# Kernel optimization log

Hardware: AMD Instinct MI355X
Metric: run time of the kernel (lower is better)

Reference implementation:

```python
import jax, jax.numpy as jnp
import numpy as np

DIM = 16
NUM_SPECIES = 10
CUTOFF = 5.0
NUM_CONVS = 3
N_ATM = 131072
N_BND = 1048576
N_ANG = 2097152
N_GRAPHS = 256
PI = 3.141592653589793


def _bessel(x, end, num_basis):
    # Sinusoidal (Bessel) radial basis on (0, end]. x: [E] -> [E, num_basis]
    xx = x[:, None] + 1e-5
    n = jnp.arange(1, num_basis + 1, dtype=x.dtype)
    return jnp.sqrt(2.0 / end) * jnp.sin(n * PI * xx / end) / xx


def _gaussian(x, start, end, num_basis):
    centers = jnp.linspace(start, end, num_basis).astype(x.dtype)
    gamma = 1.0 / (centers[1] - centers[0])
    return jnp.exp(-(gamma * (x[:, None] - centers)) ** 2)


def _ln(x, g, b):
    mu = jnp.mean(x, -1, keepdims=True)
    var = jnp.var(x, -1, keepdims=True)
    return (x - mu) * jax.lax.rsqrt(var + 1e-5) * g + b


def _embed(feat, W1, b1, W2, b2, g, b):
    # MLP([in, dim, dim], SiLU) + LayerNorm
    h = jax.nn.silu(feat @ W1 + b1)
    return _ln(h @ W2 + b2, g, b)


def _egconv(x, e, src, dst, W, bvec, lnp):
    # Edge-gated graph convolution (ALIGNN layer).
    # W: [5, D, D] = (W_src, W_dst, W_e, W_self, W_nbr); bvec: [2, D]; lnp: [2, 2, D]
    z = x[src] @ W[0] + x[dst] @ W[1] + e @ W[2] + bvec[0]  # [E, D]
    sigma = jax.nn.sigmoid(z)
    msg = sigma * (x[src] @ W[4])
    num = jax.ops.segment_sum(msg, dst, num_segments=x.shape[0])
    den = jax.ops.segment_sum(sigma, dst, num_segments=x.shape[0])
    x_new = x + jax.nn.silu(_ln(x @ W[3] + bvec[1] + num / (den + 1e-5), lnp[0, 0], lnp[0, 1]))
    e_new = e + jax.nn.silu(_ln(z, lnp[1, 0], lnp[1, 1]))
    return x_new, e_new


def _forward(x_atm, x_bnd, x_ang, mask_dih_ang, edge_index_G, edge_index_A, x_atm_batch,
             forcepair, enc_W1, enc_b1, enc_W2, enc_b2, enc_ln_g, enc_ln_b,
             conv_W, conv_b, conv_ln, l1_W, l1_b, l2_W, l2_b):
    # ---- Encoder ----
    # atom species one-hot, zero-padded from NUM_SPECIES to DIM columns (extra W rows unused)
    atm_feat = jax.nn.one_hot(x_atm, DIM, dtype=enc_W1.dtype)
    h_atm = _embed(atm_feat, enc_W1[0], enc_b1[0], enc_W2[0], enc_b2[0], enc_ln_g[0], enc_ln_b[0])
    h_bnd = _embed(_bessel(x_bnd, CUTOFF, DIM), enc_W1[1], enc_b1[1], enc_W2[1], enc_b2[1], enc_ln_g[1], enc_ln_b[1])
    h_ang_b = _embed(_gaussian(x_ang, 0.0, PI, DIM), enc_W1[2], enc_b1[2], enc_W2[2], enc_b2[2], enc_ln_g[2], enc_ln_b[2])
    h_ang_d = _embed(_gaussian(x_ang, -PI, PI, DIM), enc_W1[3], enc_b1[3], enc_W2[3], enc_b2[3], enc_ln_g[3], enc_ln_b[3])
    h_ang = jnp.where(mask_dih_ang[:, None], h_ang_d, h_ang_b)  # dihedral=True branch
    # ---- Processor: interleaved line-graph / atom-graph edge-gated convs ----
    srcA, dstA = edge_index_A[0], edge_index_A[1]
    srcG, dstG = edge_index_G[0], edge_index_G[1]
    for c in range(NUM_CONVS):
        h_bnd, h_ang = _egconv(h_bnd, h_ang, srcA, dstA, conv_W[c, 0], conv_b[c, 0], conv_ln[c, 0])
        h_atm, h_bnd = _egconv(h_atm, h_bnd, srcG, dstG, conv_W[c, 1], conv_b[c, 1], conv_ln[c, 1])
    # ---- Decoder: sum-pool atoms per graph ----
    h_pooled = jax.ops.segment_sum(h_atm, x_atm_batch, num_segments=N_GRAPHS)  # [G, D]
    # ---- Head ----
    x = jnp.concatenate([h_pooled, forcepair.reshape(N_GRAPHS, 2)], axis=-1)  # [G, D+2]
    x = jax.nn.leaky_relu(x @ l1_W + l1_b, negative_slope=0.01)
    return x @ l2_W + l2_b  # [G, 1]


def setup_inputs() -> dict:
    key = jax.random.key(0)
    ks = jax.random.split(key, 16)
    f32 = jnp.float32
    s = 0.25
    inp = {}
    inp["x_atm"] = jax.random.randint(ks[0], (N_ATM,), 0, NUM_SPECIES)
    inp["x_bnd"] = jax.random.uniform(ks[1], (N_BND,), f32, 0.5, CUTOFF)
    inp["x_ang"] = jax.random.uniform(ks[2], (N_ANG,), f32, -PI, PI)
    inp["mask_dih_ang"] = jax.random.randint(ks[3], (N_ANG,), 0, 2).astype(bool)
    inp["edge_index_G"] = jax.random.randint(ks[4], (2, N_BND), 0, N_ATM)
    inp["edge_index_A"] = jax.random.randint(ks[5], (2, N_ANG), 0, N_BND)
    inp["x_atm_batch"] = jnp.sort(jax.random.randint(ks[6], (N_ATM,), 0, N_GRAPHS))
    inp["forcepair"] = jax.random.normal(ks[7], (N_GRAPHS * 2,), f32)
    inp["enc_W1"] = jax.random.normal(ks[8], (4, DIM, DIM), f32) * s
    inp["enc_b1"] = jnp.zeros((4, DIM), f32)
    inp["enc_W2"] = jax.random.normal(ks[9], (4, DIM, DIM), f32) * s
    inp["enc_b2"] = jnp.zeros((4, DIM), f32)
    inp["enc_ln_g"] = jnp.ones((4, DIM), f32)
    inp["enc_ln_b"] = jnp.zeros((4, DIM), f32)
    inp["conv_W"] = jax.random.normal(ks[10], (NUM_CONVS, 2, 5, DIM, DIM), f32) * s
    inp["conv_b"] = jnp.zeros((NUM_CONVS, 2, 2, DIM), f32)
    inp["conv_ln"] = jnp.stack([jnp.ones((NUM_CONVS, 2, 2, DIM), f32), jnp.zeros((NUM_CONVS, 2, 2, DIM), f32)], axis=3)  # [C,2,2(node/edge? no: gamma/beta at axis 3)] -> [C,2,2,2,D]
    inp["l1_W"] = jax.random.normal(ks[11], (DIM + 2, DIM), f32) * s
    inp["l1_b"] = jnp.zeros((DIM,), f32)
    inp["l2_W"] = jax.random.normal(ks[12], (DIM, 1), f32) * s
    inp["l2_b"] = jnp.zeros((1,), f32)
    return inp


def reference(x_atm, x_bnd, x_ang, mask_dih_ang, edge_index_G, edge_index_A, x_atm_batch,
              forcepair, enc_W1, enc_b1, enc_W2, enc_b2, enc_ln_g, enc_ln_b,
              conv_W, conv_b, conv_ln, l1_W, l1_b, l2_W, l2_b):
    return _forward(x_atm, x_bnd, x_ang, mask_dih_ang, edge_index_G, edge_index_A, x_atm_batch,
                    forcepair, enc_W1, enc_b1, enc_W2, enc_b2, enc_ln_g, enc_ln_b,
                    conv_W, conv_b, conv_ln, l1_W, l1_b, l2_W, l2_b)
```

## Files before the change

### kernel.cpp

```cpp
#include <hip/hip_runtime.h>
#include <hip/hip_bf16.h>

#define N_ATM 131072
#define N_BND 1048576
#define N_ANG 2097152
#define N_GRAPHS 256
#define D_SPLIT (N_BND / 2)
#define CAP_SLOTS (N_ANG / 2 + 16384)
#define PI_F 3.14159265358979323846f

typedef __hip_bfloat16 bf16;

__device__ __forceinline__ int clampi(int v, int lo, int hi) {
    return v < lo ? lo : (v > hi ? hi : v);
}
__device__ __forceinline__ float b2f(bf16 v) { return __bfloat162float(v); }
__device__ __forceinline__ float sigmoidf_(float x) { return 1.0f / (1.0f + __expf(-x)); }
__device__ __forceinline__ float siluf_(float x) { return x / (1.0f + __expf(-x)); }

__device__ __forceinline__ float loadF(const void* p, long long i, int isbf) {
    return isbf ? b2f(((const bf16*)p)[i]) : ((const float*)p)[i];
}
__device__ __forceinline__ float bfbits2f(unsigned lo16) {
    union { unsigned u; float f; } c; c.u = lo16 << 16; return c.f;
}
__device__ __forceinline__ unsigned f2bfbits(float f) {
    union { float f; unsigned u; } c; c.f = f;
    unsigned u = c.u + 0x7FFFu + ((c.u >> 16) & 1u);
    return u >> 16;
}

__device__ __forceinline__ void load16f(const float* p, float* r) {
    const float4* q = (const float4*)p;
#pragma unroll
    for (int i = 0; i < 4; i++) { float4 v = q[i]; r[4*i]=v.x; r[4*i+1]=v.y; r[4*i+2]=v.z; r[4*i+3]=v.w; }
}
__device__ __forceinline__ void store16f(float* p, const float* r) {
    float4* q = (float4*)p;
#pragma unroll
    for (int i = 0; i < 4; i++) q[i] = make_float4(r[4*i], r[4*i+1], r[4*i+2], r[4*i+3]);
}
__device__ __forceinline__ void load16b(const bf16* p, float* r) {
    uint4 a = ((const uint4*)p)[0];
    uint4 b = ((const uint4*)p)[1];
    unsigned w[8] = {a.x, a.y, a.z, a.w, b.x, b.y, b.z, b.w};
#pragma unroll
    for (int i = 0; i < 8; i++) {
        r[2*i] = bfbits2f(w[i] & 0xFFFFu);
        union { unsigned u; float f; } c; c.u = w[i] & 0xFFFF0000u;
        r[2*i+1] = c.f;
    }
}
__device__ __forceinline__ void store16b(bf16* p, const float* r) {
    unsigned w[8];
#pragma unroll
    for (int i = 0; i < 8; i++)
        w[i] = f2bfbits(r[2*i]) | (f2bfbits(r[2*i+1]) << 16);
    ((uint4*)p)[0] = make_uint4(w[0], w[1], w[2], w[3]);
    ((uint4*)p)[1] = make_uint4(w[4], w[5], w[6], w[7]);
}

__global__ void __launch_bounds__(256) k_zero_int(int* __restrict__ p, int n) {
    int i = blockIdx.x * 256 + threadIdx.x;
    if (i < n) p[i] = 0;
}

__global__ void __launch_bounds__(256) k_detect(const void* lng, const unsigned* __restrict__ mask,
                                                int* flags) {
    int i = blockIdx.x * 256 + threadIdx.x;
    if (i == 0) flags[0] = (*(const unsigned*)lng == 0x3F803F80u) ? 1 : 0;
    int bad = 0;
    for (int j = i; j < 512 * 1024; j += 512 * 256)
        if (mask[j] > 1u) bad = 1;
    if (bad) atomicOr(&flags[1], 1);
}

__global__ void k_cvt_any(const void* __restrict__ src, float* __restrict__ dst, int n,
                          const int* __restrict__ flags) {
    int i = blockIdx.x * blockDim.x + threadIdx.x;
    if (i < n) dst[i] = loadF(src, i, flags[0]);
}

__global__ void __launch_bounds__(256) k_count(const int* __restrict__ dst, int* __restrict__ cnt,
                                               int E, int n) {
    int i = blockIdx.x * 256 + threadIdx.x;
    if (i >= E) return;
    atomicAdd(&cnt[clampi(dst[i], 0, n - 1)], 1);
}
__global__ void __launch_bounds__(256) k_scan_local(const int* __restrict__ cnt, int* __restrict__ ofs,
                                                    int* __restrict__ bsum, int n) {
    __shared__ int s[256];
    int t = threadIdx.x, i = blockIdx.x * 256 + t;
    int v = (i < n) ? cnt[i] : 0;
    s[t] = v; __syncthreads();
    for (int o = 1; o < 256; o <<= 1) {
        int add = (t >= o) ? s[t - o] : 0;
        __syncthreads();
        s[t] += add;
        __syncthreads();
    }
    if (i < n) ofs[i] = s[t] - v;
    if (t == 255) bsum[blockIdx.x] = s[255];
}
__global__ void __launch_bounds__(256) k_scan_bsum(int* __restrict__ bsum, int nb) {
    __shared__ int s[256];
    __shared__ int run;
    int t = threadIdx.x;
    if (t == 0) run = 0;
    __syncthreads();
    for (int base = 0; base < nb; base += 256) {
        int i = base + t;
        int v = (i < nb) ? bsum[i] : 0;
        s[t] = v; __syncthreads();
        for (int o = 1; o < 256; o <<= 1) {
            int add = (t >= o) ? s[t - o] : 0;
            __syncthreads();
            s[t] += add;
            __syncthreads();
        }
        if (i < nb) bsum[i] = run + s[t] - v;
        __syncthreads();
        if (t == 0) run += s[255];
        __syncthreads();
    }
}
__global__ void __launch_bounds__(256) k_scan_add(int* __restrict__ ofs, const int* __restrict__ bsum,
                                                  int* __restrict__ cursor, int n) {
    int i = blockIdx.x * 256 + threadIdx.x;
    if (i < n) { int v = ofs[i] + bsum[blockIdx.x]; ofs[i] = v; cursor[i] = v; }
}
__global__ void __launch_bounds__(256) k_scatter_line(
    const int* __restrict__ src, const int* __restrict__ dst, int* __restrict__ cur,
    int* __restrict__ srcP, int* __restrict__ dstP, int* __restrict__ pos, int E, int n)
{
    int i = blockIdx.x * 256 + threadIdx.x;
    if (i >= E) return;
    int d = clampi(dst[i], 0, n - 1);
    int s = clampi(src[i], 0, n - 1);
    int p = clampi(atomicAdd(&cur[d], 1), 0, E - 1);
    srcP[p] = s; dstP[p] = d; pos[i] = p;
}
__global__ void __launch_bounds__(256) k_scatter_pos(
    const int* __restrict__ dst, int* __restrict__ cur, int* __restrict__ pos, int E, int n)
{
    int i = blockIdx.x * 256 + threadIdx.x;
    if (i >= E) return;
    int d = clampi(dst[i], 0, n - 1);
    pos[i] = clampi(atomicAdd(&cur[d], 1), 0, E - 1);
}

__global__ void __launch_bounds__(256) k_enc_atm(
    const int* __restrict__ sp_in,
    const void* W1, const void* b1, const void* W2, const void* b2,
    const void* g, const void* be, const int* __restrict__ flags,
    float* __restrict__ out)
{
    __shared__ float sW1[256], sW2[256], sb1[16], sb2[16], sg[16], sbe[16];
    int t = threadIdx.x, isbf = flags[0];
    sW1[t] = loadF(W1, t, isbf); sW2[t] = loadF(W2, t, isbf);
    if (t < 16) { sb1[t]=loadF(b1,t,isbf); sb2[t]=loadF(b2,t,isbf); sg[t]=loadF(g,t,isbf); sbe[t]=loadF(be,t,isbf); }
    __syncthreads();
    int i = blockIdx.x * 256 + t;
    if (i >= N_ATM) return;
    int sp = clampi(sp_in[i], 0, 15);
    float h[16];
#pragma unroll
    for (int j = 0; j < 16; j++) h[j] = siluf_(sW1[sp * 16 + j] + sb1[j]);
    float o[16]; float mu = 0.f;
#pragma unroll
    for (int j = 0; j < 16; j++) {
        float a = sb2[j];
#pragma unroll
        for (int k = 0; k < 16; k++) a += h[k] * sW2[k * 16 + j];
        o[j] = a; mu += a;
    }
    mu *= (1.f / 16.f);
    float var = 0.f;
#pragma unroll
    for (int j = 0; j < 16; j++) { float d = o[j] - mu; var += d * d; }
    var *= (1.f / 16.f);
    float r = rsqrtf(var + 1e-5f);
    float ov[16];
#pragma unroll
    for (int j = 0; j < 16; j++) ov[j] = (o[j] - mu) * r * sg[j] + sbe[j];
    store16f(out + (long long)i * 16, ov);
}

__global__ void __launch_bounds__(256) k_enc_bnd(
    const void* __restrict__ xb,
    const void* W1, const void* b1, const void* W2, const void* b2,
    const void* g, const void* be, const int* __restrict__ flags,
    bf16* __restrict__ out)
{
    __shared__ float sW1[256], sW2[256], sb1[16], sb2[16], sg[16], sbe[16];
    int t = threadIdx.x, isbf = flags[0];
    sW1[t] = loadF(W1, 256 + t, isbf); sW2[t] = loadF(W2, 256 + t, isbf);
    if (t < 16) { sb1[t]=loadF(b1,16+t,isbf); sb2[t]=loadF(b2,16+t,isbf); sg[t]=loadF(g,16+t,isbf); sbe[t]=loadF(be,16+t,isbf); }
    __syncthreads();
    int i = blockIdx.x * 256 + t;
    if (i >= N_BND) return;
    float x = loadF(xb, i, isbf) + 1e-5f;
    const float c = 0.6324555320336759f;
    float inv = c / x;
    float feat[16];
#pragma unroll
    for (int k = 0; k < 16; k++) feat[k] = __sinf((float)(k + 1) * PI_F * x * 0.2f) * inv;
    float h[16];
#pragma unroll
    for (int j = 0; j < 16; j++) {
        float a = sb1[j];
#pragma unroll
        for (int k = 0; k < 16; k++) a += feat[k] * sW1[k * 16 + j];
        h[j] = siluf_(a);
    }
    float o[16]; float mu = 0.f;
#pragma unroll
    for (int j = 0; j < 16; j++) {
        float a = sb2[j];
#pragma unroll
        for (int k = 0; k < 16; k++) a += h[k] * sW2[k * 16 + j];
        o[j] = a; mu += a;
    }
    mu *= (1.f / 16.f);
    float var = 0.f;
#pragma unroll
    for (int j = 0; j < 16; j++) { float d = o[j] - mu; var += d * d; }
    var *= (1.f / 16.f);
    float r = rsqrtf(var + 1e-5f);
    float ov[16];
#pragma unroll
    for (int j = 0; j < 16; j++) ov[j] = (o[j] - mu) * r * sg[j] + sbe[j];
    store16b(out + (long long)i * 16, ov);
}

__global__ void __launch_bounds__(256) k_enc_ang(
    const void* __restrict__ xa, const void* __restrict__ mask,
    const void* W1, const void* b1, const void* W2, const void* b2,
    const void* g, const void* be, const int* __restrict__ flags,
    const int* __restrict__ pos, bf16* __restrict__ out)
{
    __shared__ float sW1[512], sW2[512], sb1[32], sb2[32], sg[32], sbe[32];
    int t = threadIdx.x, isbf = flags[0], mbyte = flags[1];
    for (int i = t; i < 512; i += 256) { sW1[i] = loadF(W1, 512 + i, isbf); sW2[i] = loadF(W2, 512 + i, isbf); }
    if (t < 32) { sb1[t]=loadF(b1,32+t,isbf); sb2[t]=loadF(b2,32+t,isbf); sg[t]=loadF(g,32+t,isbf); sbe[t]=loadF(be,32+t,isbf); }
    __syncthreads();
    int i = blockIdx.x * 256 + t;
    if (i >= N_ANG) return;
    int m = mbyte ? (((const unsigned char*)mask)[i] != 0) : (((const int*)mask)[i] != 0);
    float x = loadF(xa, i, isbf);
    float gam = m ? 2.3873241463784303f : 4.7746482927568605f;
    float c0  = m ? -PI_F : 0.0f;
    float dc  = m ? 0.41887902047863906f : 0.20943951023931953f;
    int wo = m * 256, vo = m * 16;
    float feat[16];
#pragma unroll
    for (int k = 0; k < 16; k++) {
        float d = gam * (x - (c0 + (float)k * dc));
        feat[k] = __expf(-d * d);
    }
    float h[16];
#pragma unroll
    for (int j = 0; j < 16; j++) {
        float a = sb1[vo + j];
#pragma unroll
        for (int k = 0; k < 16; k++) a += feat[k] * sW1[wo + k * 16 + j];
        h[j] = siluf_(a);
    }
    float o[16]; float mu = 0.f;
#pragma unroll
    for (int j = 0; j < 16; j++) {
        float a = sb2[vo + j];
#pragma unroll
        for (int k = 0; k < 16; k++) a += h[k] * sW2[wo + k * 16 + j];
        o[j] = a; mu += a;
    }
    mu *= (1.f / 16.f);
    float var = 0.f;
#pragma unroll
    for (int j = 0; j < 16; j++) { float d = o[j] - mu; var += d * d; }
    var *= (1.f / 16.f);
    float r = rsqrtf(var + 1e-5f);
    float ov[16];
#pragma unroll
    for (int j = 0; j < 16; j++) ov[j] = (o[j] - mu) * r * sg[vo + j] + sbe[vo + j];
    store16b(out + (long long)clampi(pos[i], 0, N_ANG - 1) * 16, ov);
}

__device__ __forceinline__ void edge_core(
    const float* xs, const float* xd, const float* ev,
    const float* sW, const float* sB, const float* sLg, const float* sLb,
    float* eo, unsigned* wpk)
{
    float z[16], mm[16];
#pragma unroll
    for (int j = 0; j < 16; j++) { z[j] = sB[j]; mm[j] = 0.f; }
#pragma unroll
    for (int k = 0; k < 16; k++) {
        float a = xs[k], c = xd[k], q = ev[k];
#pragma unroll
        for (int j = 0; j < 16; j++) {
            z[j] += a * sW[k * 16 + j] + c * sW[256 + k * 16 + j] + q * sW[512 + k * 16 + j];
            mm[j] += a * sW[1024 + k * 16 + j];
        }
    }
    float mu = 0.f;
#pragma unroll
    for (int j = 0; j < 16; j++) mu += z[j];
    mu *= (1.f / 16.f);
    float var = 0.f;
#pragma unroll
    for (int j = 0; j < 16; j++) { float dd = z[j] - mu; var += dd * dd; }
    var *= (1.f / 16.f);
    float r = rsqrtf(var + 1e-5f);
#pragma unroll
    for (int j = 0; j < 16; j++)
        eo[j] = ev[j] + siluf_((z[j] - mu) * r * sLg[j] + sLb[j]);
#pragma unroll
    for (int i = 0; i < 8; i++) {
        float a0 = sigmoidf_(z[2*i]);
        float a1 = sigmoidf_(z[2*i+1]);
        wpk[i]     = f2bfbits(a0 * mm[2*i]) | (f2bfbits(a1 * mm[2*i+1]) << 16);
        wpk[8 + i] = f2bfbits(a0)           | (f2bfbits(a1) << 16);
    }
}

__global__ void __launch_bounds__(256) k_econv_perm(
    const bf16* __restrict__ x, bf16* __restrict__ e,
    const int* __restrict__ srcP, const int* __restrict__ dstP,
    const float* __restrict__ W, const float* __restrict__ B, const float* __restrict__ L,
    bf16* __restrict__ scratch, const int* __restrict__ loP, const int* __restrict__ hiP,
    int E, int nn)
{
    int blk0 = blockIdx.x * 256;
    int lo = loP ? *loP : 0;
    int hi = hiP ? *hiP : E;
    if (blk0 + 256 <= lo || blk0 >= hi) return;
    __shared__ float sW[1280], sB[16], sLg[16], sLb[16];
    int t = threadIdx.x;
    for (int i = t; i < 1280; i += 256) sW[i] = W[i];
    if (t < 16) { sB[t] = B[t]; sLg[t] = L[32 + t]; sLb[t] = L[48 + t]; }
    __syncthreads();
    int p = blk0 + t;
    if (p < lo || p >= hi || p >= E) return;
    int s = clampi(srcP[p], 0, nn - 1);
    int d = clampi(dstP[p], 0, nn - 1);
    float xs[16], xd[16], ev[16];
    load16b(x + (long long)s * 16, xs);
    load16b(x + (long long)d * 16, xd);
    load16b(e + (long long)p * 16, ev);
    float eo[16]; unsigned wpk[16];
    edge_core(xs, xd, ev, sW, sB, sLg, sLb, eo, wpk);
    store16b(e + (long long)p * 16, eo);
    int slot = clampi(p - lo, 0, CAP_SLOTS - 1);
    uint4* sp4 = (uint4*)(scratch + (long long)slot * 32);
    sp4[0] = make_uint4(wpk[0],  wpk[1],  wpk[2],  wpk[3]);
    sp4[1] = make_uint4(wpk[4],  wpk[5],  wpk[6],  wpk[7]);
    sp4[2] = make_uint4(wpk[8],  wpk[9],  wpk[10], wpk[11]);
    sp4[3] = make_uint4(wpk[12], wpk[13], wpk[14], wpk[15]);
}

__global__ void __launch_bounds__(256) k_econv_nat(
    const float* __restrict__ x, bf16* __restrict__ e,
    const int* __restrict__ src, const int* __restrict__ dst, const int* __restrict__ pos,
    const float* __restrict__ W, const float* __restrict__ B, const float* __restrict__ L,
    bf16* __restrict__ scratch, int E, int nn)
{
    __shared__ float sW[1280], sB[16], sLg[16], sLb[16];
    int t = threadIdx.x;
    for (int i = t; i < 1280; i += 256) sW[i] = W[i];
    if (t < 16) { sB[t] = B[t]; sLg[t] = L[32 + t]; sLb[t] = L[48 + t]; }
    __syncthreads();
    int i = blockIdx.x * 256 + t;
    if (i >= E) return;
    int s = clampi(src[i], 0, nn - 1);
    int d = clampi(dst[i], 0, nn - 1);
    float xs[16], xd[16], ev[16];
    load16f(x + (long long)s * 16, xs);
    load16f(x + (long long)d * 16, xd);
    load16b(e + (long long)i * 16, ev);
    float eo[16]; unsigned wpk[16];
    edge_core(xs, xd, ev, sW, sB, sLg, sLb, eo, wpk);
    store16b(e + (long long)i * 16, eo);
    int slot = clampi(pos[i], 0, E - 1);
    uint4* sp4 = (uint4*)(scratch + (long long)slot * 32);
    sp4[0] = make_uint4(wpk[0],  wpk[1],  wpk[2],  wpk[3]);
    sp4[1] = make_uint4(wpk[4],  wpk[5],  wpk[6],  wpk[7]);
    sp4[2] = make_uint4(wpk[8],  wpk[9],  wpk[10], wpk[11]);
    sp4[3] = make_uint4(wpk[12], wpk[13], wpk[14], wpk[15]);
}

template <typename TX>
__device__ __forceinline__ void loadRow(const TX* p, float* r);
template <> __device__ __forceinline__ void loadRow<float>(const float* p, float* r) { load16f(p, r); }
template <> __device__ __forceinline__ void loadRow<bf16>(const bf16* p, float* r) { load16b(p, r); }
template <typename TX>
__device__ __forceinline__ void storeRow(TX* p, const float* r);
template <> __device__ __forceinline__ void storeRow<float>(float* p, const float* r) { store16f(p, r); }
template <> __device__ __forceinline__ void storeRow<bf16>(bf16* p, const float* r) { store16b(p, r); }

template <typename TX>
__global__ void __launch_bounds__(256) k_nconv(
    const TX* __restrict__ xo, TX* __restrict__ xn,
    const int* __restrict__ ofs, const int* __restrict__ endo,
    const float* __restrict__ W, const float* __restrict__ B, const float* __restrict__ L,
    const bf16* __restrict__ scratch, const int* __restrict__ baseP,
    int dlo, int dhi, int Emax, int cap)
{
    __shared__ float sW[256], sB[16], sLg[16], sLb[16];
    int t = threadIdx.x;
    sW[t] = W[768 + t];
    if (t < 16) { sB[t] = B[16 + t]; sLg[t] = L[t]; sLb[t] = L[16 + t]; }
    __syncthreads();
    int d = dlo + blockIdx.x * 256 + t;
    if (d >= dhi) return;
    int base = baseP ? *baseP : 0;
    float xv[16];
    loadRow<TX>(xo + (long long)d * 16, xv);
    float num[16], den[16];
#pragma unroll
    for (int j = 0; j < 16; j++) { num[j] = 0.f; den[j] = 0.f; }
    int p0 = clampi(ofs[d], 0, Emax);
    int p1 = clampi(endo[d], p0, Emax);
    for (int p = p0; p < p1; p++) {
        int idx = clampi(p - base, 0, cap - 1);
        const uint4* q = (const uint4*)(scratch + (long long)idx * 32);
        uint4 q0 = q[0], q1 = q[1], q2 = q[2], q3 = q[3];
        unsigned w[16] = {q0.x,q0.y,q0.z,q0.w, q1.x,q1.y,q1.z,q1.w,
                          q2.x,q2.y,q2.z,q2.w, q3.x,q3.y,q3.z,q3.w};
#pragma unroll
        for (int i = 0; i < 8; i++) {
            num[2*i]   += bfbits2f(w[i] & 0xFFFFu);
            num[2*i+1] += bfbits2f(w[i] >> 16);
            den[2*i]   += bfbits2f(w[8+i] & 0xFFFFu);
            den[2*i+1] += bfbits2f(w[8+i] >> 16);
        }
    }
    float tt[16]; float mu = 0.f;
#pragma unroll
    for (int j = 0; j < 16; j++) {
        float a = sB[j] + num[j] / (den[j] + 1e-5f);
#pragma unroll
        for (int k = 0; k < 16; k++) a += xv[k] * sW[k * 16 + j];
        tt[j] = a; mu += a;
    }
    mu *= (1.f / 16.f);
    float var = 0.f;
#pragma unroll
    for (int j = 0; j < 16; j++) { float dd = tt[j] - mu; var += dd * dd; }
    var *= (1.f / 16.f);
    float r = rsqrtf(var + 1e-5f);
    float ov[16];
#pragma unroll
    for (int j = 0; j < 16; j++)
        ov[j] = xv[j] + siluf_((tt[j] - mu) * r * sLg[j] + sLb[j]);
    storeRow<TX>(xn + (long long)d * 16, ov);
}

__global__ void __launch_bounds__(256) k_pool2(
    const float* __restrict__ h, const int* __restrict__ batch, float* __restrict__ pooled)
{
    int g = blockIdx.x;
    int lo = 0, hi = N_ATM;
    while (lo < hi) { int m = (lo + hi) >> 1; if (batch[m] < g) lo = m + 1; else hi = m; }
    int s0 = lo;
    lo = 0; hi = N_ATM;
    while (lo < hi) { int m = (lo + hi) >> 1; if (batch[m] < g + 1) lo = m + 1; else hi = m; }
    int s1 = lo;
    float acc[16];
#pragma unroll
    for (int j = 0; j < 16; j++) acc[j] = 0.f;
    for (int i = s0 + threadIdx.x; i < s1; i += 256) {
        float v[16];
        load16f(h + (long long)i * 16, v);
#pragma unroll
        for (int j = 0; j < 16; j++) acc[j] += v[j];
    }
#pragma unroll
    for (int j = 0; j < 16; j++)
        for (int o = 32; o > 0; o >>= 1) acc[j] += __shfl_down(acc[j], o, 64);
    __shared__ float red[4][16];
    int wv = threadIdx.x >> 6, ln = threadIdx.x & 63;
    if (ln == 0)
#pragma unroll
        for (int j = 0; j < 16; j++) red[wv][j] = acc[j];
    __syncthreads();
    if (threadIdx.x < 16)
        pooled[g * 16 + threadIdx.x] = red[0][threadIdx.x] + red[1][threadIdx.x]
                                     + red[2][threadIdx.x] + red[3][threadIdx.x];
}

__global__ void __launch_bounds__(256) k_head(
    const float* __restrict__ pooled, const void* __restrict__ fp,
    const void* l1W, const void* l1b, const void* l2W, const void* l2b,
    const int* __restrict__ flags, void* __restrict__ out)
{
    __shared__ float sW[18 * 16], sb[16], s2W[16];
    int t = threadIdx.x, isbf = flags[0];
    for (int i = t; i < 288; i += 256) sW[i] = loadF(l1W, i, isbf);
    if (t < 16) { sb[t] = loadF(l1b, t, isbf); s2W[t] = loadF(l2W, t, isbf); }
    __syncthreads();
    int g = t;
    if (g >= N_GRAPHS) return;
    float in[18];
#pragma unroll
    for (int j = 0; j < 16; j++) in[j] = pooled[g * 16 + j];
    in[16] = loadF(fp, 2 * g, isbf);
    in[17] = loadF(fp, 2 * g + 1, isbf);
    float acc = loadF(l2b, 0, isbf);
#pragma unroll
    for (int j = 0; j < 16; j++) {
        float h = sb[j];
#pragma unroll
        for (int k = 0; k < 18; k++) h += in[k] * sW[k * 16 + j];
        h = (h > 0.f) ? h : 0.01f * h;
        acc += h * s2W[j];
    }
    if (isbf) ((bf16*)out)[g] = __float2bfloat16(acc);
    else      ((float*)out)[g] = acc;
}

extern "C" void kernel_launch(void* const* d_in, const int* in_sizes, int n_in,
                              void* d_out, int out_size, void* d_ws, size_t ws_size,
                              hipStream_t stream) {
    const int*  x_atm = (const int*)d_in[0];
    const void* x_bnd = d_in[1];
    const void* x_ang = d_in[2];
    const void* mask  = d_in[3];
    const int*  eiG   = (const int*)d_in[4];
    const int*  eiA   = (const int*)d_in[5];
    const int*  batch = (const int*)d_in[6];
    const void* fp    = d_in[7];
    const void* eW1 = d_in[8],  *eb1 = d_in[9],  *eW2 = d_in[10], *eb2 = d_in[11];
    const void* elg = d_in[12], *elb = d_in[13];
    const void* convW = d_in[14], *convB = d_in[15], *convLN = d_in[16];
    const void* l1W = d_in[17], *l1b = d_in[18], *l2W = d_in[19], *l2b = d_in[20];

    const size_t NA16 = (size_t)N_ATM * 16;
    const size_t NB16 = (size_t)N_BND * 16;
    const size_t NG16 = (size_t)N_ANG * 16;

    char* p = (char*)d_ws;
    int*   flags  = (int*)p;   p += 256;
    float* cw     = (float*)p; p += 7680 * 4;
    float* cb     = (float*)p; p += 192 * 4;
    float* cln    = (float*)p; p += 384 * 4;
    float* pooled = (float*)p; p += 4096 * 4;
    int*   bsum   = (int*)p;   p += 4096 * 4;
    int*   cntB   = (int*)p;   p += (size_t)N_BND * 4;
    int*   ofsB   = (int*)p;   p += (size_t)N_BND * 4;
    int*   srcB   = (int*)p;   p += (size_t)N_ANG * 4;
    int*   dstB   = (int*)p;   p += (size_t)N_ANG * 4;
    int*   cntA   = (int*)p;   p += (size_t)N_ATM * 4;
    int*   ofsA   = (int*)p;   p += (size_t)N_ATM * 4;
    int*   posG   = (int*)p;   p += (size_t)N_BND * 4;
    float* h_atm  = (float*)p; p += NA16 * 4;
    bf16*  h_bndX = (bf16*)p;  p += NB16 * 2;
    bf16*  h_bndY = (bf16*)p;  p += NB16 * 2;
    bf16*  h_ang  = (bf16*)p;  p += NG16 * 2;
    int*   posB    = (int*)p;
    bf16*  scratch = (bf16*)p;

    k_zero_int<<<1, 64, 0, stream>>>(flags, 64);
    k_detect<<<512, 256, 0, stream>>>(elg, (const unsigned*)mask, flags);
    k_cvt_any<<<30, 256, 0, stream>>>(convW, cw, 7680, flags);
    k_cvt_any<<<1, 256, 0, stream>>>(convB, cb, 192, flags);
    k_cvt_any<<<2, 256, 0, stream>>>(convLN, cln, 384, flags);

    k_zero_int<<<N_BND / 256, 256, 0, stream>>>(cntB, N_BND);
    k_count<<<N_ANG / 256, 256, 0, stream>>>(eiA + N_ANG, cntB, N_ANG, N_BND);
    k_scan_local<<<N_BND / 256, 256, 0, stream>>>(cntB, ofsB, bsum, N_BND);
    k_scan_bsum<<<1, 256, 0, stream>>>(bsum, N_BND / 256);
    k_scan_add<<<N_BND / 256, 256, 0, stream>>>(ofsB, bsum, cntB, N_BND);
    k_scatter_line<<<N_ANG / 256, 256, 0, stream>>>(eiA, eiA + N_ANG, cntB, srcB, dstB, posB,
                                                    N_ANG, N_BND);
    k_zero_int<<<N_ATM / 256, 256, 0, stream>>>(cntA, N_ATM);
    k_count<<<N_BND / 256, 256, 0, stream>>>(eiG + N_BND, cntA, N_BND, N_ATM);
    k_scan_local<<<N_ATM / 256, 256, 0, stream>>>(cntA, ofsA, bsum, N_ATM);
    k_scan_bsum<<<1, 256, 0, stream>>>(bsum, N_ATM / 256);
    k_scan_add<<<N_ATM / 256, 256, 0, stream>>>(ofsA, bsum, cntA, N_ATM);
    k_scatter_pos<<<N_BND / 256, 256, 0, stream>>>(eiG + N_BND, cntA, posG, N_BND, N_ATM);

    k_enc_atm<<<N_ATM / 256, 256, 0, stream>>>(x_atm, eW1, eb1, eW2, eb2, elg, elb, flags, h_atm);
    k_enc_bnd<<<N_BND / 256, 256, 0, stream>>>(x_bnd, eW1, eb1, eW2, eb2, elg, elb, flags, h_bndX);
    k_enc_ang<<<N_ANG / 256, 256, 0, stream>>>(x_ang, mask, eW1, eb1, eW2, eb2, elg, elb, flags,
                                               posB, h_ang);

    bf16* X = h_bndX;
    bf16* Y = h_bndY;
    const int* split = ofsB + D_SPLIT;
    for (int c = 0; c < 3; c++) {
        const float* Wl = cw + (size_t)(c * 2 + 0) * 1280;
        const float* Bl = cb + (size_t)(c * 2 + 0) * 32;
        const float* Ll = cln + (size_t)(c * 2 + 0) * 64;
        k_econv_perm<<<N_ANG / 256, 256, 0, stream>>>(X, h_ang, srcB, dstB, Wl, Bl, Ll,
                                                      scratch, (const int*)nullptr, split,
                                                      N_ANG, N_BND);
        k_nconv<bf16><<<D_SPLIT / 256, 256, 0, stream>>>(X, Y, ofsB, cntB, Wl, Bl, Ll,
                                                         scratch, (const int*)nullptr,
                                                         0, D_SPLIT, N_ANG, CAP_SLOTS);
        k_econv_perm<<<N_ANG / 256, 256, 0, stream>>>(X, h_ang, srcB, dstB, Wl, Bl, Ll,
                                                      scratch, split, (const int*)nullptr,
                                                      N_ANG, N_BND);
        k_nconv<bf16><<<(N_BND - D_SPLIT) / 256, 256, 0, stream>>>(X, Y, ofsB, cntB, Wl, Bl, Ll,
                                                                   scratch, split,
                                                                   D_SPLIT, N_BND, N_ANG, CAP_SLOTS);
        const float* Wa = cw + (size_t)(c * 2 + 1) * 1280;
        const float* Ba = cb + (size_t)(c * 2 + 1) * 32;
        const float* La = cln + (size_t)(c * 2 + 1) * 64;
        k_econv_nat<<<N_BND / 256, 256, 0, stream>>>(h_atm, Y, eiG, eiG + N_BND, posG,
                                                     Wa, Ba, La, scratch, N_BND, N_ATM);
        k_nconv<float><<<N_ATM / 256, 256, 0, stream>>>(h_atm, h_atm, ofsA, cntA, Wa, Ba, La,
                                                        scratch, (const int*)nullptr,
                                                        0, N_ATM, N_BND, N_BND);
        bf16* tmp = X; X = Y; Y = tmp;
    }

    k_pool2<<<N_GRAPHS, 256, 0, stream>>>(h_atm, batch, pooled);
    k_head<<<1, 256, 0, stream>>>(pooled, fp, l1W, l1b, l2W, l2b, flags, d_out);
}
```

Before: 2.537 ms.

## Fuse edge and node convolution into one CSR-windowed kernel with shared-memory messages

Replaces the separate edge-conv and node-aggregation kernels with one fused kernel per conv. Each block handles a window of 256 destination-sorted edges (plus up to 64 extension edges), stages the packed sigma-message pairs in shared memory, and reduces them into the destination nodes it owns. This removes the global scratch round trip and the half-split launches. The atom graph now uses a CSR permutation with an edge-id indirection, which makes the bond-feature accesses indirect. Nodes with more incoming edges than the window's extension can hold would be aggregated incorrectly, and the owner/first ranges need extra binary-search setup kernels.

```diff
diff --git a/kernel.cpp b/kernel.cpp
--- a/kernel.cpp
+++ b/kernel.cpp
@@ -5,9 +5,11 @@
 #define N_BND 1048576
 #define N_ANG 2097152
 #define N_GRAPHS 256
-#define D_SPLIT (N_BND / 2)
-#define CAP_SLOTS (N_ANG / 2 + 16384)
 #define PI_F 3.14159265358979323846f
+
+#define FMAIN 256
+#define FEXT 64
+#define FWIN (FMAIN + FEXT)
 
 typedef __hip_bfloat16 bf16;
 
@@ -59,6 +61,15 @@
     ((uint4*)p)[0] = make_uint4(w[0], w[1], w[2], w[3]);
     ((uint4*)p)[1] = make_uint4(w[4], w[5], w[6], w[7]);
 }
+
+template <typename TX>
+__device__ __forceinline__ void loadRow(const TX* p, float* r);
+template <> __device__ __forceinline__ void loadRow<float>(const float* p, float* r) { load16f(p, r); }
+template <> __device__ __forceinline__ void loadRow<bf16>(const bf16* p, float* r) { load16b(p, r); }
+template <typename TX>
+__device__ __forceinline__ void storeRow(TX* p, const float* r);
+template <> __device__ __forceinline__ void storeRow<float>(float* p, const float* r) { store16f(p, r); }
+template <> __device__ __forceinline__ void storeRow<bf16>(bf16* p, const float* r) { store16b(p, r); }
 
 __global__ void __launch_bounds__(256) k_zero_int(int* __restrict__ p, int n) {
     int i = blockIdx.x * 256 + threadIdx.x;
@@ -124,29 +135,45 @@
         __syncthreads();
     }
 }
-__global__ void __launch_bounds__(256) k_scan_add(int* __restrict__ ofs, const int* __restrict__ bsum,
-                                                  int* __restrict__ cursor, int n) {
+__global__ void __launch_bounds__(256) k_scan_add2(int* __restrict__ ofs, const int* __restrict__ bsum,
+                                                   int* __restrict__ cursor, int n, int total) {
     int i = blockIdx.x * 256 + threadIdx.x;
     if (i < n) { int v = ofs[i] + bsum[blockIdx.x]; ofs[i] = v; cursor[i] = v; }
-}
-__global__ void __launch_bounds__(256) k_scatter_line(
+    if (i == 0) ofs[n] = total;
+}
+__global__ void __launch_bounds__(256) k_scatter_line2(
     const int* __restrict__ src, const int* __restrict__ dst, int* __restrict__ cur,
-    int* __restrict__ srcP, int* __restrict__ dstP, int* __restrict__ pos, int E, int n)
+    int* __restrict__ srcP, int* __restrict__ pos, int E, int n)
 {
     int i = blockIdx.x * 256 + threadIdx.x;
     if (i >= E) return;
     int d = clampi(dst[i], 0, n - 1);
     int s = clampi(src[i], 0, n - 1);
     int p = clampi(atomicAdd(&cur[d], 1), 0, E - 1);
-    srcP[p] = s; dstP[p] = d; pos[i] = p;
-}
-__global__ void __launch_bounds__(256) k_scatter_pos(
-    const int* __restrict__ dst, int* __restrict__ cur, int* __restrict__ pos, int E, int n)
+    srcP[p] = s; pos[i] = p;
+}
+__global__ void __launch_bounds__(256) k_scatter_atom2(
+    const int* __restrict__ src, const int* __restrict__ dst, int* __restrict__ cur,
+    int* __restrict__ srcP, int* __restrict__ eidP, int E, int n, int ns)
 {
     int i = blockIdx.x * 256 + threadIdx.x;
     if (i >= E) return;
     int d = clampi(dst[i], 0, n - 1);
-    pos[i] = clampi(atomicAdd(&cur[d], 1), 0, E - 1);
+    int s = clampi(src[i], 0, ns - 1);
+    int p = clampi(atomicAdd(&cur[d], 1), 0, E - 1);
+    srcP[p] = s; eidP[p] = i;
+}
+__global__ void __launch_bounds__(256) k_blkrange(const int* __restrict__ ofs, int N, int nbp1,
+                                                  int* __restrict__ owner, int* __restrict__ first) {
+    int b = blockIdx.x * 256 + threadIdx.x;
+    if (b >= nbp1) return;
+    int B0 = b * FMAIN;
+    int lo = 0, hi = N;
+    while (lo < hi) { int m = (lo + hi) >> 1; if (ofs[m] < B0) lo = m + 1; else hi = m; }
+    first[b] = lo;
+    lo = 0; hi = N + 1;
+    while (lo < hi) { int m = (lo + hi) >> 1; if (ofs[m] <= B0) lo = m + 1; else hi = m; }
+    owner[b] = (lo - 1) < 0 ? 0 : (lo - 1);
 }
 
 __global__ void __launch_bounds__(256) k_enc_atm(
@@ -324,136 +351,112 @@
     }
 }
 
-__global__ void __launch_bounds__(256) k_econv_perm(
-    const bf16* __restrict__ x, bf16* __restrict__ e,
-    const int* __restrict__ srcP, const int* __restrict__ dstP,
-    const float* __restrict__ W, const float* __restrict__ B, const float* __restrict__ L,
-    bf16* __restrict__ scratch, const int* __restrict__ loP, const int* __restrict__ hiP,
-    int E, int nn)
-{
-    int blk0 = blockIdx.x * 256;
-    int lo = loP ? *loP : 0;
-    int hi = hiP ? *hiP : E;
-    if (blk0 + 256 <= lo || blk0 >= hi) return;
-    __shared__ float sW[1280], sB[16], sLg[16], sLb[16];
+template <typename TX, bool VIA_EID>
+__global__ void __launch_bounds__(256) k_fused(
+    const TX* __restrict__ X, TX* __restrict__ Xn,
+    const bf16* __restrict__ Ein, bf16* __restrict__ Eout,
+    const int* __restrict__ src, const int* __restrict__ eid,
+    const int* __restrict__ ofs, const int* __restrict__ owner, const int* __restrict__ first,
+    const float* __restrict__ W, const float* __restrict__ Bp, const float* __restrict__ L,
+    int E, int N, int nb)
+{
+    __shared__ float sW[1280], sB[32], sLg[32], sLb[32];
+    __shared__ unsigned sMS[FWIN * 17];
+    __shared__ int sDst[FWIN];
     int t = threadIdx.x;
+    int b = blockIdx.x;
+    int B0 = b * FMAIN;
     for (int i = t; i < 1280; i += 256) sW[i] = W[i];
-    if (t < 16) { sB[t] = B[t]; sLg[t] = L[32 + t]; sLb[t] = L[48 + t]; }
-    __syncthreads();
-    int p = blk0 + t;
-    if (p < lo || p >= hi || p >= E) return;
-    int s = clampi(srcP[p], 0, nn - 1);
-    int d = clampi(dstP[p], 0, nn - 1);
-    float xs[16], xd[16], ev[16];
-    load16b(x + (long long)s * 16, xs);
-    load16b(x + (long long)d * 16, xd);
-    load16b(e + (long long)p * 16, ev);
-    float eo[16]; unsigned wpk[16];
-    edge_core(xs, xd, ev, sW, sB, sLg, sLb, eo, wpk);
-    store16b(e + (long long)p * 16, eo);
-    int slot = clampi(p - lo, 0, CAP_SLOTS - 1);
-    uint4* sp4 = (uint4*)(scratch + (long long)slot * 32);
-    sp4[0] = make_uint4(wpk[0],  wpk[1],  wpk[2],  wpk[3]);
-    sp4[1] = make_uint4(wpk[4],  wpk[5],  wpk[6],  wpk[7]);
-    sp4[2] = make_uint4(wpk[8],  wpk[9],  wpk[10], wpk[11]);
-    sp4[3] = make_uint4(wpk[12], wpk[13], wpk[14], wpk[15]);
-}
-
-__global__ void __launch_bounds__(256) k_econv_nat(
-    const float* __restrict__ x, bf16* __restrict__ e,
-    const int* __restrict__ src, const int* __restrict__ dst, const int* __restrict__ pos,
-    const float* __restrict__ W, const float* __restrict__ B, const float* __restrict__ L,
-    bf16* __restrict__ scratch, int E, int nn)
-{
-    __shared__ float sW[1280], sB[16], sLg[16], sLb[16];
-    int t = threadIdx.x;
-    for (int i = t; i < 1280; i += 256) sW[i] = W[i];
-    if (t < 16) { sB[t] = B[t]; sLg[t] = L[32 + t]; sLb[t] = L[48 + t]; }
-    __syncthreads();
-    int i = blockIdx.x * 256 + t;
-    if (i >= E) return;
-    int s = clampi(src[i], 0, nn - 1);
-    int d = clampi(dst[i], 0, nn - 1);
-    float xs[16], xd[16], ev[16];
-    load16f(x + (long long)s * 16, xs);
-    load16f(x + (long long)d * 16, xd);
-    load16b(e + (long long)i * 16, ev);
-    float eo[16]; unsigned wpk[16];
-    edge_core(xs, xd, ev, sW, sB, sLg, sLb, eo, wpk);
-    store16b(e + (long long)i * 16, eo);
-    int slot = clampi(pos[i], 0, E - 1);
-    uint4* sp4 = (uint4*)(scratch + (long long)slot * 32);
-    sp4[0] = make_uint4(wpk[0],  wpk[1],  wpk[2],  wpk[3]);
-    sp4[1] = make_uint4(wpk[4],  wpk[5],  wpk[6],  wpk[7]);
-    sp4[2] = make_uint4(wpk[8],  wpk[9],  wpk[10], wpk[11]);
-    sp4[3] = make_uint4(wpk[12], wpk[13], wpk[14], wpk[15]);
-}
-
-template <typename TX>
-__device__ __forceinline__ void loadRow(const TX* p, float* r);
-template <> __device__ __forceinline__ void loadRow<float>(const float* p, float* r) { load16f(p, r); }
-template <> __device__ __forceinline__ void loadRow<bf16>(const bf16* p, float* r) { load16b(p, r); }
-template <typename TX>
-__device__ __forceinline__ void storeRow(TX* p, const float* r);
-template <> __device__ __forceinline__ void storeRow<float>(float* p, const float* r) { store16f(p, r); }
-template <> __device__ __forceinline__ void storeRow<bf16>(bf16* p, const float* r) { store16b(p, r); }
-
-template <typename TX>
-__global__ void __launch_bounds__(256) k_nconv(
-    const TX* __restrict__ xo, TX* __restrict__ xn,
-    const int* __restrict__ ofs, const int* __restrict__ endo,
-    const float* __restrict__ W, const float* __restrict__ B, const float* __restrict__ L,
-    const bf16* __restrict__ scratch, const int* __restrict__ baseP,
-    int dlo, int dhi, int Emax, int cap)
-{
-    __shared__ float sW[256], sB[16], sLg[16], sLb[16];
-    int t = threadIdx.x;
-    sW[t] = W[768 + t];
-    if (t < 16) { sB[t] = B[16 + t]; sLg[t] = L[t]; sLb[t] = L[16 + t]; }
-    __syncthreads();
-    int d = dlo + blockIdx.x * 256 + t;
-    if (d >= dhi) return;
-    int base = baseP ? *baseP : 0;
-    float xv[16];
-    loadRow<TX>(xo + (long long)d * 16, xv);
-    float num[16], den[16];
-#pragma unroll
-    for (int j = 0; j < 16; j++) { num[j] = 0.f; den[j] = 0.f; }
-    int p0 = clampi(ofs[d], 0, Emax);
-    int p1 = clampi(endo[d], p0, Emax);
-    for (int p = p0; p < p1; p++) {
-        int idx = clampi(p - base, 0, cap - 1);
-        const uint4* q = (const uint4*)(scratch + (long long)idx * 32);
-        uint4 q0 = q[0], q1 = q[1], q2 = q[2], q3 = q[3];
-        unsigned w[16] = {q0.x,q0.y,q0.z,q0.w, q1.x,q1.y,q1.z,q1.w,
-                          q2.x,q2.y,q2.z,q2.w, q3.x,q3.y,q3.z,q3.w};
-#pragma unroll
-        for (int i = 0; i < 8; i++) {
-            num[2*i]   += bfbits2f(w[i] & 0xFFFFu);
-            num[2*i+1] += bfbits2f(w[i] >> 16);
-            den[2*i]   += bfbits2f(w[8+i] & 0xFFFFu);
-            den[2*i+1] += bfbits2f(w[8+i] >> 16);
+    if (t < 16) {
+        sB[t] = Bp[t];        sB[16 + t] = Bp[16 + t];
+        sLg[t] = L[32 + t];   sLb[t] = L[48 + t];
+        sLg[16 + t] = L[t];   sLb[16 + t] = L[16 + t];
+    }
+    int d0      = owner[b];
+    int dNodeLo = first[b];
+    int dhi     = first[b + 1];
+    int dhiN    = (b == nb - 1) ? N : dhi;
+    for (int dd = d0 + t; dd < dhi; dd += 256) {
+        int a = ofs[dd], e2 = ofs[dd + 1];
+        int lo2 = a < B0 ? B0 : a;
+        int hi2 = e2 > B0 + FWIN ? B0 + FWIN : e2;
+        for (int p = lo2; p < hi2; p++) sDst[p - B0] = dd;
+    }
+    __syncthreads();
+    {
+        int p = B0 + t;
+        int s = clampi(src[p], 0, N - 1);
+        int d = clampi(sDst[t], 0, N - 1);
+        long long erow = VIA_EID ? (long long)clampi(eid[p], 0, E - 1) : (long long)p;
+        float xs[16], xd[16], ev[16];
+        loadRow<TX>(X + (long long)s * 16, xs);
+        loadRow<TX>(X + (long long)d * 16, xd);
+        load16b(Ein + erow * 16, ev);
+        float eo[16]; unsigned wpk[16];
+        edge_core(xs, xd, ev, sW, sB, sLg, sLb, eo, wpk);
+        store16b(Eout + erow * 16, eo);
+        unsigned* ms = &sMS[t * 17];
+#pragma unroll
+        for (int i = 0; i < 16; i++) ms[i] = wpk[i];
+    }
+    int endW = ofs[clampi(dhi, 0, N)];
+    int eExt = endW - (B0 + FMAIN);
+    eExt = eExt < 0 ? 0 : (eExt > FEXT ? FEXT : eExt);
+    if (t < eExt) {
+        int p = B0 + FMAIN + t;
+        int s = clampi(src[p], 0, N - 1);
+        int d = clampi(dhi - 1, 0, N - 1);
+        long long erow = VIA_EID ? (long long)clampi(eid[p], 0, E - 1) : (long long)p;
+        float xs[16], xd[16], ev[16];
+        loadRow<TX>(X + (long long)s * 16, xs);
+        loadRow<TX>(X + (long long)d * 16, xd);
+        load16b(Ein + erow * 16, ev);
+        float eo[16]; unsigned wpk[16];
+        edge_core(xs, xd, ev, sW, sB, sLg, sLb, eo, wpk);
+        unsigned* ms = &sMS[(FMAIN + t) * 17];
+#pragma unroll
+        for (int i = 0; i < 16; i++) ms[i] = wpk[i];
+    }
+    __syncthreads();
+    for (int d = dNodeLo + t; d < dhiN; d += 256) {
+        float xv[16];
+        loadRow<TX>(X + (long long)d * 16, xv);
+        float num[16], den[16];
+#pragma unroll
+        for (int j = 0; j < 16; j++) { num[j] = 0.f; den[j] = 0.f; }
+        int p0 = ofs[d], p1 = ofs[d + 1];
+        for (int p = p0; p < p1; p++) {
+            int q = clampi(p - B0, 0, FWIN - 1);
+            const unsigned* ms = &sMS[q * 17];
+#pragma unroll
+            for (int i = 0; i < 8; i++) {
+                unsigned w0 = ms[i], w1 = ms[8 + i];
+                num[2*i]   += bfbits2f(w0 & 0xFFFFu);
+                num[2*i+1] += bfbits2f(w0 >> 16);
+                den[2*i]   += bfbits2f(w1 & 0xFFFFu);
+                den[2*i+1] += bfbits2f(w1 >> 16);
+            }
         }
-    }
-    float tt[16]; float mu = 0.f;
-#pragma unroll
-    for (int j = 0; j < 16; j++) {
-        float a = sB[j] + num[j] / (den[j] + 1e-5f);
-#pragma unroll
-        for (int k = 0; k < 16; k++) a += xv[k] * sW[k * 16 + j];
-        tt[j] = a; mu += a;
-    }
-    mu *= (1.f / 16.f);
-    float var = 0.f;
-#pragma unroll
-    for (int j = 0; j < 16; j++) { float dd = tt[j] - mu; var += dd * dd; }
-    var *= (1.f / 16.f);
-    float r = rsqrtf(var + 1e-5f);
-    float ov[16];
-#pragma unroll
-    for (int j = 0; j < 16; j++)
-        ov[j] = xv[j] + siluf_((tt[j] - mu) * r * sLg[j] + sLb[j]);
-    storeRow<TX>(xn + (long long)d * 16, ov);
+        float tt[16]; float mu = 0.f;
+#pragma unroll
+        for (int j = 0; j < 16; j++) {
+            float a = sB[16 + j] + num[j] / (den[j] + 1e-5f);
+#pragma unroll
+            for (int k = 0; k < 16; k++) a += xv[k] * sW[768 + k * 16 + j];
+            tt[j] = a; mu += a;
+        }
+        mu *= (1.f / 16.f);
+        float var = 0.f;
+#pragma unroll
+        for (int j = 0; j < 16; j++) { float dd2 = tt[j] - mu; var += dd2 * dd2; }
+        var *= (1.f / 16.f);
+        float r = rsqrtf(var + 1e-5f);
+        float ov[16];
+#pragma unroll
+        for (int j = 0; j < 16; j++)
+            ov[j] = xv[j] + siluf_((tt[j] - mu) * r * sLg[16 + j] + sLb[16 + j]);
+        storeRow<TX>(Xn + (long long)d * 16, ov);
+    }
 }
 
 __global__ void __launch_bounds__(256) k_pool2(
@@ -535,9 +538,8 @@
     const void* convW = d_in[14], *convB = d_in[15], *convLN = d_in[16];
     const void* l1W = d_in[17], *l1b = d_in[18], *l2W = d_in[19], *l2b = d_in[20];
 
-    const size_t NA16 = (size_t)N_ATM * 16;
-    const size_t NB16 = (size_t)N_BND * 16;
-    const size_t NG16 = (size_t)N_ANG * 16;
+    const int NB_L = N_ANG / FMAIN;
+    const int NB_A = N_BND / FMAIN;
 
     char* p = (char*)d_ws;
     int*   flags  = (int*)p;   p += 256;
@@ -546,19 +548,24 @@
     float* cln    = (float*)p; p += 384 * 4;
     float* pooled = (float*)p; p += 4096 * 4;
     int*   bsum   = (int*)p;   p += 4096 * 4;
-    int*   cntB   = (int*)p;   p += (size_t)N_BND * 4;
-    int*   ofsB   = (int*)p;   p += (size_t)N_BND * 4;
+    int*   ownerL = (int*)p;   p += 8448 * 4;
+    int*   firstL = (int*)p;   p += 8448 * 4;
+    int*   ownerA = (int*)p;   p += 4352 * 4;
+    int*   firstA = (int*)p;   p += 4352 * 4;
+    int*   ofsB   = (int*)p;   p += (size_t)(N_BND + 256) * 4;
     int*   srcB   = (int*)p;   p += (size_t)N_ANG * 4;
-    int*   dstB   = (int*)p;   p += (size_t)N_ANG * 4;
-    int*   cntA   = (int*)p;   p += (size_t)N_ATM * 4;
-    int*   ofsA   = (int*)p;   p += (size_t)N_ATM * 4;
-    int*   posG   = (int*)p;   p += (size_t)N_BND * 4;
-    float* h_atm  = (float*)p; p += NA16 * 4;
-    bf16*  h_bndX = (bf16*)p;  p += NB16 * 2;
-    bf16*  h_bndY = (bf16*)p;  p += NB16 * 2;
-    bf16*  h_ang  = (bf16*)p;  p += NG16 * 2;
-    int*   posB    = (int*)p;
-    bf16*  scratch = (bf16*)p;
+    int*   ofsA   = (int*)p;   p += (size_t)(N_ATM + 256) * 4;
+    int*   srcG   = (int*)p;   p += (size_t)N_BND * 4;
+    int*   eidG   = (int*)p;   p += (size_t)N_BND * 4;
+    float* atmA   = (float*)p; p += (size_t)N_ATM * 64;
+    float* atmB   = (float*)p; p += (size_t)N_ATM * 64;
+    bf16*  bndA   = (bf16*)p;  p += (size_t)N_BND * 32;
+    bf16*  bndB   = (bf16*)p;  p += (size_t)N_BND * 32;
+    bf16*  angA   = (bf16*)p;  p += (size_t)N_ANG * 32;
+    bf16*  angB   = (bf16*)p;
+    int*   curB   = (int*)bndB;
+    int*   curA   = curB + N_BND;
+    int*   posB   = curA + N_ATM;
 
     k_zero_int<<<1, 64, 0, stream>>>(flags, 64);
     k_detect<<<512, 256, 0, stream>>>(elg, (const unsigned*)mask, flags);
@@ -566,55 +573,48 @@
     k_cvt_any<<<1, 256, 0, stream>>>(convB, cb, 192, flags);
     k_cvt_any<<<2, 256, 0, stream>>>(convLN, cln, 384, flags);
 
-    k_zero_int<<<N_BND / 256, 256, 0, stream>>>(cntB, N_BND);
-    k_count<<<N_ANG / 256, 256, 0, stream>>>(eiA + N_ANG, cntB, N_ANG, N_BND);
-    k_scan_local<<<N_BND / 256, 256, 0, stream>>>(cntB, ofsB, bsum, N_BND);
+    k_zero_int<<<N_BND / 256, 256, 0, stream>>>(curB, N_BND);
+    k_count<<<N_ANG / 256, 256, 0, stream>>>(eiA + N_ANG, curB, N_ANG, N_BND);
+    k_scan_local<<<N_BND / 256, 256, 0, stream>>>(curB, ofsB, bsum, N_BND);
     k_scan_bsum<<<1, 256, 0, stream>>>(bsum, N_BND / 256);
-    k_scan_add<<<N_BND / 256, 256, 0, stream>>>(ofsB, bsum, cntB, N_BND);
-    k_scatter_line<<<N_ANG / 256, 256, 0, stream>>>(eiA, eiA + N_ANG, cntB, srcB, dstB, posB,
-                                                    N_ANG, N_BND);
-    k_zero_int<<<N_ATM / 256, 256, 0, stream>>>(cntA, N_ATM);
-    k_count<<<N_BND / 256, 256, 0, stream>>>(eiG + N_BND, cntA, N_BND, N_ATM);
-    k_scan_local<<<N_ATM / 256, 256, 0, stream>>>(cntA, ofsA, bsum, N_ATM);
+    k_scan_add2<<<N_BND / 256, 256, 0, stream>>>(ofsB, bsum, curB, N_BND, N_ANG);
+    k_scatter_line2<<<N_ANG / 256, 256, 0, stream>>>(eiA, eiA + N_ANG, curB, srcB, posB,
+                                                     N_ANG, N_BND);
+    k_blkrange<<<(NB_L + 256) / 256, 256, 0, stream>>>(ofsB, N_BND, NB_L + 1, ownerL, firstL);
+
+    k_zero_int<<<N_ATM / 256, 256, 0, stream>>>(curA, N_ATM);
+    k_count<<<N_BND / 256, 256, 0, stream>>>(eiG + N_BND, curA, N_BND, N_ATM);
+    k_scan_local<<<N_ATM / 256, 256, 0, stream>>>(curA, ofsA, bsum, N_ATM);
     k_scan_bsum<<<1, 256, 0, stream>>>(bsum, N_ATM / 256);
-    k_scan_add<<<N_ATM / 256, 256, 0, stream>>>(ofsA, bsum, cntA, N_ATM);
-    k_scatter_pos<<<N_BND / 256, 256, 0, stream>>>(eiG + N_BND, cntA, posG, N_BND, N_ATM);
-
-    k_enc_atm<<<N_ATM / 256, 256, 0, stream>>>(x_atm, eW1, eb1, eW2, eb2, elg, elb, flags, h_atm);
-    k_enc_bnd<<<N_BND / 256, 256, 0, stream>>>(x_bnd, eW1, eb1, eW2, eb2, elg, elb, flags, h_bndX);
+    k_scan_add2<<<N_ATM / 256, 256, 0, stream>>>(ofsA, bsum, curA, N_ATM, N_BND);
+    k_scatter_atom2<<<N_BND / 256, 256, 0, stream>>>(eiG, eiG + N_BND, curA, srcG, eidG,
+                                                     N_BND, N_ATM, N_ATM);
+    k_blkrange<<<(NB_A + 256) / 256, 256, 0, stream>>>(ofsA, N_ATM, NB_A + 1, ownerA, firstA);
+
+    k_enc_atm<<<N_ATM / 256, 256, 0, stream>>>(x_atm, eW1, eb1, eW2, eb2, elg, elb, flags, atmA);
+    k_enc_bnd<<<N_BND / 256, 256, 0, stream>>>(x_bnd, eW1, eb1, eW2, eb2, elg, elb, flags, bndA);
     k_enc_ang<<<N_ANG / 256, 256, 0, stream>>>(x_ang, mask, eW1, eb1, eW2, eb2, elg, elb, flags,
-                                               posB, h_ang);
-
-    bf16* X = h_bndX;
-    bf16* Y = h_bndY;
-    const int* split = ofsB + D_SPLIT;
+                                               posB, angA);
+
+    float* atmCur = atmA; float* atmOth = atmB;
+    bf16*  angCur = angA; bf16*  angOth = angB;
     for (int c = 0; c < 3; c++) {
         const float* Wl = cw + (size_t)(c * 2 + 0) * 1280;
         const float* Bl = cb + (size_t)(c * 2 + 0) * 32;
         const float* Ll = cln + (size_t)(c * 2 + 0) * 64;
-        k_econv_perm<<<N_ANG / 256, 256, 0, stream>>>(X, h_ang, srcB, dstB, Wl, Bl, Ll,
-                                                      scratch, (const int*)nullptr, split,
-                                                      N_ANG, N_BND);
-        k_nconv<bf16><<<D_SPLIT / 256, 256, 0, stream>>>(X, Y, ofsB, cntB, Wl, Bl, Ll,
-                                                         scratch, (const int*)nullptr,
-                                                         0, D_SPLIT, N_ANG, CAP_SLOTS);
-        k_econv_perm<<<N_ANG / 256, 256, 0, stream>>>(X, h_ang, srcB, dstB, Wl, Bl, Ll,
-                                                      scratch, split, (const int*)nullptr,
-                                                      N_ANG, N_BND);
-        k_nconv<bf16><<<(N_BND - D_SPLIT) / 256, 256, 0, stream>>>(X, Y, ofsB, cntB, Wl, Bl, Ll,
-                                                                   scratch, split,
-                                                                   D_SPLIT, N_BND, N_ANG, CAP_SLOTS);
+        k_fused<bf16, false><<<NB_L, 256, 0, stream>>>(
+            bndA, bndB, angCur, angOth, srcB, (const int*)nullptr,
+            ofsB, ownerL, firstL, Wl, Bl, Ll, N_ANG, N_BND, NB_L);
         const float* Wa = cw + (size_t)(c * 2 + 1) * 1280;
         const float* Ba = cb + (size_t)(c * 2 + 1) * 32;
         const float* La = cln + (size_t)(c * 2 + 1) * 64;
-        k_econv_nat<<<N_BND / 256, 256, 0, stream>>>(h_atm, Y, eiG, eiG + N_BND, posG,
-                                                     Wa, Ba, La, scratch, N_BND, N_ATM);
-        k_nconv<float><<<N_ATM / 256, 256, 0, stream>>>(h_atm, h_atm, ofsA, cntA, Wa, Ba, La,
-                                                        scratch, (const int*)nullptr,
-                                                        0, N_ATM, N_BND, N_BND);
-        bf16* tmp = X; X = Y; Y = tmp;
-    }
-
-    k_pool2<<<N_GRAPHS, 256, 0, stream>>>(h_atm, batch, pooled);
+        k_fused<float, true><<<NB_A, 256, 0, stream>>>(
+            atmCur, atmOth, bndB, bndA, srcG, eidG,
+            ofsA, ownerA, firstA, Wa, Ba, La, N_BND, N_ATM, NB_A);
+        float* ft = atmCur; atmCur = atmOth; atmOth = ft;
+        bf16*  bt = angCur; angCur = angOth; angOth = bt;
+    }
+
+    k_pool2<<<N_GRAPHS, 256, 0, stream>>>(atmCur, batch, pooled);
     k_head<<<1, 256, 0, stream>>>(pooled, fp, l1W, l1b, l2W, l2b, flags, d_out);
 }
```

Measured after the change: 6.248 ms. 2.46x slower.
